# Kernel tuning notes

Measured on AMD Instinct MI355X. Metric: run time of the kernel, lower is better.

The kernel has to match this reference:

```python
import jax, jax.numpy as jnp
import numpy as np

B, L, K, H = 512, 512, 103, 512
I = K + 2  # LSTM input = obs(103) + fed-back pos(2)


def setup_inputs() -> dict:
    key = jax.random.key(0)
    ks = jax.random.split(key, 14)
    s = 0.02
    return {
        "x": jax.random.normal(ks[0], (B, L, K), dtype=jnp.float32),
        "pos": jax.random.normal(ks[1], (B, L, 2), dtype=jnp.float32),
        "hidden_state": jnp.zeros((B, H), dtype=jnp.float32),
        "cell_state": jnp.zeros((B, H), dtype=jnp.float32),
        # LSTM params (PyTorch layout: gates ordered i,f,g,o)
        "W_ih": jax.random.normal(ks[2], (4 * H, I), dtype=jnp.float32) * s,
        "W_hh": jax.random.normal(ks[3], (4 * H, H), dtype=jnp.float32) * s,
        "b_ih": jnp.zeros((4 * H,), dtype=jnp.float32),
        "b_hh": jnp.zeros((4 * H,), dtype=jnp.float32),
        # MLP: H -> 64 -> 16 -> 2, all ReLU
        "W1": jax.random.normal(ks[4], (64, H), dtype=jnp.float32) * s,
        "b1": jnp.zeros((64,), dtype=jnp.float32),
        "W2": jax.random.normal(ks[5], (16, 64), dtype=jnp.float32) * s,
        "b2": jnp.zeros((16,), dtype=jnp.float32),
        "W3": jax.random.normal(ks[6], (2, 16), dtype=jnp.float32) * s,
        "b3": jnp.zeros((2,), dtype=jnp.float32),
    }


def reference(x, pos, hidden_state, cell_state, W_ih, W_hh, b_ih, b_hh,
              W1, b1, W2, b2, W3, b3):
    b = b_ih + b_hh

    def step(carry, x_t):
        h, c, ip = carry  # (B,H),(B,H),(B,2)
        inp = jnp.concatenate([x_t, ip], axis=-1)  # (B, I)
        gates = inp @ W_ih.T + h @ W_hh.T + b      # (B, 4H)
        i, f, g, o = jnp.split(gates, 4, axis=-1)
        c = jax.nn.sigmoid(f) * c + jax.nn.sigmoid(i) * jnp.tanh(g)
        h = jax.nn.sigmoid(o) * jnp.tanh(c)
        y = jax.nn.relu(h @ W1.T + b1)
        y = jax.nn.relu(y @ W2.T + b2)
        y = jax.nn.relu(y @ W3.T + b3)  # (B,2) predicted next pos
        return (h, c, y), y

    xs = jnp.swapaxes(x, 0, 1)  # (L,B,K)
    (h, c, _), ys = jax.lax.scan(step, (hidden_state, cell_state, pos[:, 0, :]), xs)
    predicted_pos = jnp.swapaxes(ys, 0, 1)  # (B,L,2)
    return predicted_pos, h, c
```

## Files before the change

### kernel.cpp

```cpp
#include <hip/hip_runtime.h>

#define NB 512
#define NL 512
#define NK 103
#define NH 512
#define NI 105
#define XROW (NL * NK)

typedef _Float16 half8 __attribute__((ext_vector_type(8)));
typedef _Float16 half4 __attribute__((ext_vector_type(4)));
typedef float floatx4 __attribute__((ext_vector_type(4)));

union U16 { half8 h; unsigned long long u[2]; };

#define XB_STR 136
#define B2_STR 136
#define YST_STR 72
#define Y2_STR 16
#define OFF_XB  0
#define OFF_B2  34816
#define OFF_YST 52224
#define OFF_Y2  61440
#define OFF_FR  63488
#define SMEM_BYTES 65280

#define SPIN_MAX (1 << 20)

#define A_LOAD(p)  __hip_atomic_load((p),  __ATOMIC_RELAXED, __HIP_MEMORY_SCOPE_AGENT)
#define A_STORE(p, v) __hip_atomic_store((p), (v), __ATOMIC_RELAXED, __HIP_MEMORY_SCOPE_AGENT)


__device__ __forceinline__ float fast_sigmoid(float v) {
  v = fminf(fmaxf(v, -30.f), 30.f);
  return __builtin_amdgcn_rcpf(1.f + __expf(-v));
}
__device__ __forceinline__ float fast_tanh(float v) {
  v = fminf(fmaxf(v, -15.f), 15.f);
  float e = __expf(-2.f * v);
  return (1.f - e) * __builtin_amdgcn_rcpf(1.f + e);
}

__global__ void __launch_bounds__(256, 1)
lstm_persist(const float* __restrict__ x, const float* __restrict__ pos,
             const float* __restrict__ h0, const float* __restrict__ c0,
             const float* __restrict__ Wih, const float* __restrict__ Whh,
             const float* __restrict__ bih, const float* __restrict__ bhh,
             const float* __restrict__ W1, const float* __restrict__ b1,
             const float* __restrict__ W2, const float* __restrict__ b2,
             const float* __restrict__ W3, const float* __restrict__ b3,
             float* __restrict__ out, void* __restrict__ ws)
{
  extern __shared__ char smem[];
  _Float16* B2s = (_Float16*)(smem + OFF_B2);
  _Float16* YST = (_Float16*)(smem + OFF_YST);
  _Float16* Y2  = (_Float16*)(smem + OFF_Y2);
  _Float16* HTX = Y2;
  float* FR  = (float*)(smem + OFF_FR);
  float* b1s = FR;
  float* b2s = FR + 64;
  float* w3s = FR + 80;
  float* b3s = FR + 112;
  float* wy0 = FR + 114;
  float* wy1 = FR + 178;
  float* bgs = FR + 242;
  float* ypres = FR + 306;
  volatile int* abflag = (volatile int*)(FR + 440);

  const int tid = threadIdx.x;
  const int g  = blockIdx.x >> 5;
  const int cs = blockIdx.x & 31;
  const int w  = tid >> 6, l = tid & 63;
  const int c16 = l & 15, q = l >> 4;
  const int rh = w >> 1;
  const int ch = w & 1;

  unsigned* flags = (unsigned*)ws;
  char* hbase = (char*)ws + 4096;

  if (tid == 0) *abflag = 0;
  {
    unsigned* xz = (unsigned*)(smem + OFF_XB);
    for (int i = tid; i < 8704; i += 256) xz[i] = 0;
  }
  for (int idx = tid; idx < 64 * 128; idx += 256) {
    int cc = idx >> 7, k = idx & 127;
    int gr = (cc >> 4) * NH + cs * 16 + (cc & 15);
    float v = (k < NK) ? Wih[(size_t)gr * NI + k] : 0.f;
    B2s[cc * B2_STR + k] = (_Float16)v;
  }
  if (tid < 64) {
    int gr = (tid >> 4) * NH + cs * 16 + (tid & 15);
    wy0[tid] = Wih[(size_t)gr * NI + 103];
    wy1[tid] = Wih[(size_t)gr * NI + 104];
    bgs[tid] = bih[gr] + bhh[gr];
    b1s[tid] = b1[tid];
  }
  if (tid < 16) b2s[tid] = b2[tid];
  if (tid < 32) w3s[tid] = W3[tid];
  if (tid < 2)  b3s[tid] = b3[tid];

  {
    const int r = tid >> 2, hb = tid & 3;
    const float* src = h0 + (size_t)(64 * g + r) * NH + cs * 16 + hb * 4;
    union { unsigned long long u; half4 h; } cv;
    cv.h[0] = (_Float16)src[0]; cv.h[1] = (_Float16)src[1];
    cv.h[2] = (_Float16)src[2]; cv.h[3] = (_Float16)src[3];
    A_STORE((unsigned long long*)(hbase + (size_t)cs * 16384
                                  + (size_t)(64 * g + r) * 32 + hb * 8), cv.u);
  }

  half8 bfr[4][16];
  #pragma unroll
  for (int ct = 0; ct < 4; ++ct) {
    const int rown = ch ? (ct * 16 + c16) : (ct * NH + cs * 16 + c16);
    const float* rp = (ch ? W1 : Whh) + (size_t)rown * NH;
    #pragma unroll
    for (int kk = 0; kk < 16; ++kk) {
      const float* p = rp + kk * 32 + q * 8;
      floatx4 f0 = *(const floatx4*)(p);
      floatx4 f1 = *(const floatx4*)(p + 4);
      half8 hv;
      hv[0]=(_Float16)f0[0]; hv[1]=(_Float16)f0[1]; hv[2]=(_Float16)f0[2]; hv[3]=(_Float16)f0[3];
      hv[4]=(_Float16)f1[0]; hv[5]=(_Float16)f1[1]; hv[6]=(_Float16)f1[2]; hv[7]=(_Float16)f1[3];
      bfr[ct][kk] = hv;
    }
  }
  half8 w2f[2];
  if (ch) {
    #pragma unroll
    for (int kk = 0; kk < 2; ++kk) {
      const float* p = W2 + c16 * 64 + kk * 32 + q * 8;
      floatx4 f0 = *(const floatx4*)(p);
      floatx4 f1 = *(const floatx4*)(p + 4);
      half8 hv;
      hv[0]=(_Float16)f0[0]; hv[1]=(_Float16)f0[1]; hv[2]=(_Float16)f0[2]; hv[3]=(_Float16)f0[3];
      hv[4]=(_Float16)f1[0]; hv[5]=(_Float16)f1[1]; hv[6]=(_Float16)f1[2]; hv[7]=(_Float16)f1[3];
      w2f[kk] = hv;
    }
  }
  float cacc[2][4];
  if (!ch) {
    #pragma unroll
    for (int rt = 0; rt < 2; ++rt)
      #pragma unroll
      for (int reg = 0; reg < 4; ++reg)
        cacc[rt][reg] = c0[(size_t)(64 * g + 32 * rh + 16 * rt + q * 4 + reg) * NH + cs * 16 + c16];
  }

  auto xstage = [&](int t1) {
    _Float16* xb = (_Float16*)(smem + OFF_XB) + (size_t)(t1 & 1) * 64 * XB_STR;
    const int row = 32 * rh + (l >> 1);
    const int p = l & 1;
    const float* src = x + (size_t)(64 * g + row) * XROW + (size_t)t1 * NK + p * 52;
    _Float16* dst = xb + row * XB_STR + p * 52;
    const int nfull = p ? 12 : 13;
    for (int cnk = 0; cnk < nfull; ++cnk) {
      float f0 = src[cnk * 4 + 0], f1 = src[cnk * 4 + 1];
      float f2 = src[cnk * 4 + 2], f3 = src[cnk * 4 + 3];
      half4 hv; hv[0]=(_Float16)f0; hv[1]=(_Float16)f1; hv[2]=(_Float16)f2; hv[3]=(_Float16)f3;
      *(half4*)(dst + cnk * 4) = hv;
    }
    if (p) {
      dst[48] = (_Float16)src[48];
      dst[49] = (_Float16)src[49];
      dst[50] = (_Float16)src[50];
    }
  };

  auto fpub = [&](unsigned val) {
    if (tid == 0) A_STORE(flags + ((g << 5) + cs) * 4, val);
  };

  __syncthreads();
  if (!ch) xstage(0);
  __syncthreads();
  fpub(1);

  for (int t = 0; t <= NL; ++t) {
    if (l < 32) {
      unsigned* f = flags + ((g << 5) + l) * 4;
      int spins = 0;
      while (A_LOAD(f) < (unsigned)(t + 1)) {
        if (++spins > SPIN_MAX) { *abflag = 1; break; }
      }
    }

    U16 ar[2][16];
    {
      const char* lb = hbase + (size_t)(t & 1) * 524288
                     + (size_t)(q >> 1) * 16384
                     + (size_t)(64 * g + 32 * rh + c16) * 32 + (q & 1) * 16;
      #pragma unroll
      for (int kk = 0; kk < 16; ++kk) {
        #pragma unroll
        for (int rt = 0; rt < 2; ++rt) {
          const unsigned long long* up =
              (const unsigned long long*)(lb + (size_t)kk * 32768 + rt * 512);
          ar[rt][kk].u[0] = A_LOAD(up);
          ar[rt][kk].u[1] = A_LOAD(up + 1);
        }
      }
    }

    floatx4 acc[4][2] = {};

    if (!ch && t < NL) {
      const _Float16* xb = (const _Float16*)(smem + OFF_XB) + (size_t)(t & 1) * 64 * XB_STR;
      #pragma unroll
      for (int kb = 0; kb < 4; ++kb) {
        half8 ax[2];
        #pragma unroll
        for (int rt = 0; rt < 2; ++rt)
          ax[rt] = *(const half8*)(xb + (32 * rh + 16 * rt + c16) * XB_STR + kb * 32 + q * 8);
        #pragma unroll
        for (int ct = 0; ct < 4; ++ct) {
          half8 bf = *(const half8*)(B2s + (ct * 16 + c16) * B2_STR + kb * 32 + q * 8);
          #pragma unroll
          for (int rt = 0; rt < 2; ++rt)
            acc[ct][rt] = __builtin_amdgcn_mfma_f32_16x16x32_f16(ax[rt], bf, acc[ct][rt], 0, 0, 0);
        }
      }
      if (t + 1 < NL) xstage(t + 1);
    }

    #pragma unroll
    for (int kk = 0; kk < 16; ++kk)
      #pragma unroll
      for (int ct = 0; ct < 4; ++ct) {
        acc[ct][0] = __builtin_amdgcn_mfma_f32_16x16x32_f16(ar[0][kk].h, bfr[ct][kk], acc[ct][0], 0, 0, 0);
        acc[ct][1] = __builtin_amdgcn_mfma_f32_16x16x32_f16(ar[1][kk].h, bfr[ct][kk], acc[ct][1], 0, 0, 0);
      }

    if (ch) {
      if (t == 0) {
        if (l < 32) {
          int row = 32 * rh + l;
          const float* pp = pos + (size_t)(64 * g + row) * (NL * 2);
          ypres[row * 2 + 0] = pp[0];
          ypres[row * 2 + 1] = pp[1];
        }
      } else {
        #pragma unroll
        for (int ct = 0; ct < 4; ++ct)
          #pragma unroll
          for (int rt = 0; rt < 2; ++rt)
            #pragma unroll
            for (int reg = 0; reg < 4; ++reg) {
              int row = 32 * rh + 16 * rt + q * 4 + reg;
              float v = acc[ct][rt][reg] + b1s[ct * 16 + c16];
              YST[row * YST_STR + ct * 16 + c16] = (_Float16)fmaxf(v, 0.f);
            }
        floatx4 a2c[2] = {};
        #pragma unroll
        for (int kk2 = 0; kk2 < 2; ++kk2)
          #pragma unroll
          for (int rt = 0; rt < 2; ++rt) {
            half8 af = *(const half8*)(YST + (32 * rh + 16 * rt + c16) * YST_STR + kk2 * 32 + q * 8);
            a2c[rt] = __builtin_amdgcn_mfma_f32_16x16x32_f16(af, w2f[kk2], a2c[rt], 0, 0, 0);
          }
        #pragma unroll
        for (int rt = 0; rt < 2; ++rt)
          #pragma unroll
          for (int reg = 0; reg < 4; ++reg) {
            int row = 32 * rh + 16 * rt + q * 4 + reg;
            float v = a2c[rt][reg] + b2s[c16];
            Y2[row * Y2_STR + c16] = (_Float16)fmaxf(v, 0.f);
          }
        if (l < 32) {
          int row = 32 * rh + l;
          float y0 = b3s[0], y1 = b3s[1];
          #pragma unroll
          for (int k = 0; k < 16; ++k) {
            float vv = (float)Y2[row * Y2_STR + k];
            y0 += vv * w3s[k];
            y1 += vv * w3s[16 + k];
          }
          y0 = fmaxf(y0, 0.f); y1 = fmaxf(y1, 0.f);
          ypres[row * 2 + 0] = y0;
          ypres[row * 2 + 1] = y1;
          if (cs == 0) {
            float2* op = (float2*)(out + (size_t)(64 * g + row) * (NL * 2) + (size_t)(t - 1) * 2);
            *op = make_float2(y0, y1);
          }
        }
      }
    }
    __syncthreads();
    if (*abflag) return;

    if (!ch && t < NL) {
      #pragma unroll
      for (int rt = 0; rt < 2; ++rt)
        #pragma unroll
        for (int reg = 0; reg < 4; ++reg) {
          int rl = 32 * rh + 16 * rt + q * 4 + reg;
          float yp0 = ypres[rl * 2], yp1 = ypres[rl * 2 + 1];
          float gi = acc[0][rt][reg] + bgs[c16]      + yp0 * wy0[c16]      + yp1 * wy1[c16];
          float gf = acc[1][rt][reg] + bgs[16 + c16] + yp0 * wy0[16 + c16] + yp1 * wy1[16 + c16];
          float gg = acc[2][rt][reg] + bgs[32 + c16] + yp0 * wy0[32 + c16] + yp1 * wy1[32 + c16];
          float go = acc[3][rt][reg] + bgs[48 + c16] + yp0 * wy0[48 + c16] + yp1 * wy1[48 + c16];
          float iv = fast_sigmoid(gi);
          float fv = fast_sigmoid(gf);
          float gv = fast_tanh(gg);
          float ov = fast_sigmoid(go);
          float cn = fv * cacc[rt][reg] + iv * gv;
          cacc[rt][reg] = cn;
          float hn = ov * fast_tanh(cn);
          HTX[rl * 16 + c16] = (_Float16)hn;
          if (t == NL - 1) {
            out[(size_t)(NB * NL * 2) + (size_t)(64 * g + rl) * NH + cs * 16 + c16] = hn;
            out[(size_t)(NB * NL * 2) + (size_t)(NB * NH) + (size_t)(64 * g + rl) * NH + cs * 16 + c16] = cn;
          }
        }
    }

    if (t < NL) {
      __syncthreads();
      {
        const int r = tid >> 2, hb = tid & 3;
        char* dst = hbase + (size_t)((t + 1) & 1) * 524288
                  + (size_t)cs * 16384 + (size_t)(64 * g + r) * 32 + hb * 8;
        unsigned long long v = *(const unsigned long long*)(HTX + r * 16 + hb * 4);
        A_STORE((unsigned long long*)dst, v);
      }
      __syncthreads();
      fpub((unsigned)(t + 2));
    }
  }
}

extern "C" void kernel_launch(void* const* d_in, const int* in_sizes, int n_in,
                              void* d_out, int out_size, void* d_ws, size_t ws_size,
                              hipStream_t stream) {
  (void)in_sizes; (void)n_in; (void)out_size; (void)ws_size;
  const float* x   = (const float*)d_in[0];
  const float* pos = (const float*)d_in[1];
  const float* h0  = (const float*)d_in[2];
  const float* c0  = (const float*)d_in[3];
  const float* Wih = (const float*)d_in[4];
  const float* Whh = (const float*)d_in[5];
  const float* bih = (const float*)d_in[6];
  const float* bhh = (const float*)d_in[7];
  const float* W1  = (const float*)d_in[8];
  const float* b1  = (const float*)d_in[9];
  const float* W2  = (const float*)d_in[10];
  const float* b2  = (const float*)d_in[11];
  const float* W3  = (const float*)d_in[12];
  const float* b3  = (const float*)d_in[13];
  float* out = (float*)d_out;

  hipMemsetAsync(d_ws, 0, 4096, stream);

  void* args[] = { (void*)&x, (void*)&pos, (void*)&h0, (void*)&c0,
                   (void*)&Wih, (void*)&Whh, (void*)&bih, (void*)&bhh,
                   (void*)&W1, (void*)&b1, (void*)&W2, (void*)&b2,
                   (void*)&W3, (void*)&b3, (void*)&out, (void*)&d_ws };

  hipError_t err = hipLaunchCooperativeKernel(
      reinterpret_cast<void*>(lstm_persist),
      dim3(256, 1, 1), dim3(256, 1, 1), args, (unsigned)SMEM_BYTES, stream);
  if (err != hipSuccess) {
    (void)hipGetLastError();
    lstm_persist<<<dim3(256, 1, 1), dim3(256, 1, 1), SMEM_BYTES, stream>>>(
        x, pos, h0, c0, Wih, Whh, bih, bhh, W1, b1, W2, b2, W3, b3, out, d_ws);
  }
}
```

Baseline: 5.453 ms.

## Split LSTM batch into 32-row groups, split-K hidden matmul across wave pairs

Doubles the persistent grid to 512 blocks, each handling 32 batch rows instead of 64, so each block group's per-step work shrinks. Within a block, two waves split the K dimension of the recurrent and W1 matmuls and combine their partial sums through new shared-memory reduction buffers (GG, GM). Publishing h and the step flag now happens from a single wave with an explicit vmcnt wait instead of two extra block barriers. The cost is more blocks spinning on flags, an extra shared-memory reduction per step, and reliance on two blocks fitting per CU for the cooperative launch.

```diff
diff --git a/kernel.cpp b/kernel.cpp
--- a/kernel.cpp
+++ b/kernel.cpp
@@ -16,13 +16,15 @@
 #define XB_STR 136
 #define B2_STR 136
 #define YST_STR 72
-#define Y2_STR 16
 #define OFF_XB  0
-#define OFF_B2  34816
-#define OFF_YST 52224
-#define OFF_Y2  61440
-#define OFF_FR  63488
-#define SMEM_BYTES 65280
+#define OFF_B2  17408
+#define OFF_YST 34816
+#define OFF_Y2  39424
+#define OFF_HTX 40448
+#define OFF_GG  41472
+#define OFF_GM  50176
+#define OFF_FR  58880
+#define SMEM_BYTES 60480
 
 #define SPIN_MAX (1 << 20)
 
@@ -40,7 +42,7 @@
   return (1.f - e) * __builtin_amdgcn_rcpf(1.f + e);
 }
 
-__global__ void __launch_bounds__(256, 1)
+__global__ void __launch_bounds__(256, 2)
 lstm_persist(const float* __restrict__ x, const float* __restrict__ pos,
              const float* __restrict__ h0, const float* __restrict__ c0,
              const float* __restrict__ Wih, const float* __restrict__ Whh,
@@ -54,7 +56,9 @@
   _Float16* B2s = (_Float16*)(smem + OFF_B2);
   _Float16* YST = (_Float16*)(smem + OFF_YST);
   _Float16* Y2  = (_Float16*)(smem + OFF_Y2);
-  _Float16* HTX = Y2;
+  _Float16* HTX = (_Float16*)(smem + OFF_HTX);
+  float* GG = (float*)(smem + OFF_GG);
+  float* GM = (float*)(smem + OFF_GM);
   float* FR  = (float*)(smem + OFF_FR);
   float* b1s = FR;
   float* b2s = FR + 64;
@@ -64,23 +68,23 @@
   float* wy1 = FR + 178;
   float* bgs = FR + 242;
   float* ypres = FR + 306;
-  volatile int* abflag = (volatile int*)(FR + 440);
+  volatile int* abflag = (volatile int*)(FR + 370);
 
   const int tid = threadIdx.x;
   const int g  = blockIdx.x >> 5;
   const int cs = blockIdx.x & 31;
   const int w  = tid >> 6, l = tid & 63;
   const int c16 = l & 15, q = l >> 4;
-  const int rh = w >> 1;
-  const int ch = w & 1;
+  const int pair = w >> 1;
+  const int wv = w & 1;
 
   unsigned* flags = (unsigned*)ws;
-  char* hbase = (char*)ws + 4096;
+  char* hbase = (char*)ws + 8192;
 
   if (tid == 0) *abflag = 0;
   {
     unsigned* xz = (unsigned*)(smem + OFF_XB);
-    for (int i = tid; i < 8704; i += 256) xz[i] = 0;
+    for (int i = tid; i < 4352; i += 256) xz[i] = 0;
   }
   for (int idx = tid; idx < 64 * 128; idx += 256) {
     int cc = idx >> 7, k = idx & 127;
@@ -99,24 +103,24 @@
   if (tid < 32) w3s[tid] = W3[tid];
   if (tid < 2)  b3s[tid] = b3[tid];
 
-  {
+  if (tid < 128) {
     const int r = tid >> 2, hb = tid & 3;
-    const float* src = h0 + (size_t)(64 * g + r) * NH + cs * 16 + hb * 4;
+    const float* src = h0 + (size_t)(32 * g + r) * NH + cs * 16 + hb * 4;
     union { unsigned long long u; half4 h; } cv;
     cv.h[0] = (_Float16)src[0]; cv.h[1] = (_Float16)src[1];
     cv.h[2] = (_Float16)src[2]; cv.h[3] = (_Float16)src[3];
     A_STORE((unsigned long long*)(hbase + (size_t)cs * 16384
-                                  + (size_t)(64 * g + r) * 32 + hb * 8), cv.u);
-  }
-
-  half8 bfr[4][16];
+                                  + (size_t)(32 * g + r) * 32 + hb * 8), cv.u);
+  }
+
+  half8 bfr[4][8];
   #pragma unroll
   for (int ct = 0; ct < 4; ++ct) {
-    const int rown = ch ? (ct * 16 + c16) : (ct * NH + cs * 16 + c16);
-    const float* rp = (ch ? W1 : Whh) + (size_t)rown * NH;
+    const int rown = pair ? (ct * 16 + c16) : (ct * NH + cs * 16 + c16);
+    const float* rp = (pair ? W1 : Whh) + (size_t)rown * NH;
     #pragma unroll
-    for (int kk = 0; kk < 16; ++kk) {
-      const float* p = rp + kk * 32 + q * 8;
+    for (int kk = 0; kk < 8; ++kk) {
+      const float* p = rp + (wv * 8 + kk) * 32 + q * 8;
       floatx4 f0 = *(const floatx4*)(p);
       floatx4 f1 = *(const floatx4*)(p + 4);
       half8 hv;
@@ -126,7 +130,7 @@
     }
   }
   half8 w2f[2];
-  if (ch) {
+  if (w == 2) {
     #pragma unroll
     for (int kk = 0; kk < 2; ++kk) {
       const float* p = W2 + c16 * 64 + kk * 32 + q * 8;
@@ -138,20 +142,18 @@
       w2f[kk] = hv;
     }
   }
-  float cacc[2][4];
-  if (!ch) {
+  float cacc[4];
+  if (pair == 0) {
     #pragma unroll
-    for (int rt = 0; rt < 2; ++rt)
-      #pragma unroll
-      for (int reg = 0; reg < 4; ++reg)
-        cacc[rt][reg] = c0[(size_t)(64 * g + 32 * rh + 16 * rt + q * 4 + reg) * NH + cs * 16 + c16];
+    for (int reg = 0; reg < 4; ++reg)
+      cacc[reg] = c0[(size_t)(32 * g + 16 * wv + q * 4 + reg) * NH + cs * 16 + c16];
   }
 
   auto xstage = [&](int t1) {
-    _Float16* xb = (_Float16*)(smem + OFF_XB) + (size_t)(t1 & 1) * 64 * XB_STR;
-    const int row = 32 * rh + (l >> 1);
+    _Float16* xb = (_Float16*)(smem + OFF_XB) + (size_t)(t1 & 1) * 32 * XB_STR;
+    const int row = l >> 1;
     const int p = l & 1;
-    const float* src = x + (size_t)(64 * g + row) * XROW + (size_t)t1 * NK + p * 52;
+    const float* src = x + (size_t)(32 * g + row) * XROW + (size_t)t1 * NK + p * 52;
     _Float16* dst = xb + row * XB_STR + p * 52;
     const int nfull = p ? 12 : 13;
     for (int cnk = 0; cnk < nfull; ++cnk) {
@@ -167,77 +169,103 @@
     }
   };
 
-  auto fpub = [&](unsigned val) {
-    if (tid == 0) A_STORE(flags + ((g << 5) + cs) * 4, val);
-  };
-
   __syncthreads();
-  if (!ch) xstage(0);
+  if (w == 1) xstage(0);
   __syncthreads();
-  fpub(1);
+  if (tid == 0) A_STORE(flags + ((g << 5) + cs) * 4, 1u);
 
   for (int t = 0; t <= NL; ++t) {
-    if (l < 32) {
-      unsigned* f = flags + ((g << 5) + l) * 4;
-      int spins = 0;
-      while (A_LOAD(f) < (unsigned)(t + 1)) {
-        if (++spins > SPIN_MAX) { *abflag = 1; break; }
-      }
-    }
-
-    U16 ar[2][16];
-    {
-      const char* lb = hbase + (size_t)(t & 1) * 524288
-                     + (size_t)(q >> 1) * 16384
-                     + (size_t)(64 * g + 32 * rh + c16) * 32 + (q & 1) * 16;
+    floatx4 acc[4][2] = {};
+    const bool active = (pair == 1) || (t < NL);
+
+    if (active) {
+      if (l < 16) {
+        unsigned* f = flags + ((g << 5) + wv * 16 + l) * 4;
+        int spins = 0;
+        while (A_LOAD(f) < (unsigned)(t + 1)) {
+          if (++spins > SPIN_MAX) { *abflag = 1; break; }
+        }
+      }
+      U16 ar[2][8];
+      {
+        const char* lb = hbase + (size_t)(t & 1) * 524288
+                       + (size_t)wv * 262144 + (size_t)(q >> 1) * 16384
+                       + (size_t)(32 * g + c16) * 32 + (q & 1) * 16;
+        #pragma unroll
+        for (int kk = 0; kk < 8; ++kk) {
+          #pragma unroll
+          for (int rt = 0; rt < 2; ++rt) {
+            const unsigned long long* up =
+                (const unsigned long long*)(lb + (size_t)kk * 32768 + rt * 512);
+            ar[rt][kk].u[0] = A_LOAD(up);
+            ar[rt][kk].u[1] = A_LOAD(up + 1);
+          }
+        }
+      }
+
+      if (pair == 0 && t < NL) {
+        const _Float16* xb = (const _Float16*)(smem + OFF_XB) + (size_t)(t & 1) * 32 * XB_STR;
+        #pragma unroll
+        for (int kbi = 0; kbi < 2; ++kbi) {
+          const int kb = 2 * wv + kbi;
+          half8 ax[2];
+          #pragma unroll
+          for (int rt = 0; rt < 2; ++rt)
+            ax[rt] = *(const half8*)(xb + (16 * rt + c16) * XB_STR + kb * 32 + q * 8);
+          #pragma unroll
+          for (int ct = 0; ct < 4; ++ct) {
+            half8 bf = *(const half8*)(B2s + (ct * 16 + c16) * B2_STR + kb * 32 + q * 8);
+            #pragma unroll
+            for (int rt = 0; rt < 2; ++rt)
+              acc[ct][rt] = __builtin_amdgcn_mfma_f32_16x16x32_f16(ax[rt], bf, acc[ct][rt], 0, 0, 0);
+          }
+        }
+        if (w == 1 && t + 1 < NL) xstage(t + 1);
+      }
+
       #pragma unroll
-      for (int kk = 0; kk < 16; ++kk) {
-        #pragma unroll
-        for (int rt = 0; rt < 2; ++rt) {
-          const unsigned long long* up =
-              (const unsigned long long*)(lb + (size_t)kk * 32768 + rt * 512);
-          ar[rt][kk].u[0] = A_LOAD(up);
-          ar[rt][kk].u[1] = A_LOAD(up + 1);
-        }
-      }
-    }
-
-    floatx4 acc[4][2] = {};
-
-    if (!ch && t < NL) {
-      const _Float16* xb = (const _Float16*)(smem + OFF_XB) + (size_t)(t & 1) * 64 * XB_STR;
+      for (int kk = 0; kk < 8; ++kk)
+        #pragma unroll
+        for (int ct = 0; ct < 4; ++ct) {
+          acc[ct][0] = __builtin_amdgcn_mfma_f32_16x16x32_f16(ar[0][kk].h, bfr[ct][kk], acc[ct][0], 0, 0, 0);
+          acc[ct][1] = __builtin_amdgcn_mfma_f32_16x16x32_f16(ar[1][kk].h, bfr[ct][kk], acc[ct][1], 0, 0, 0);
+        }
+
+      if (pair == 0) {
+        #pragma unroll
+        for (int ct = 0; ct < 4; ++ct)
+          #pragma unroll
+          for (int reg = 0; reg < 4; ++reg)
+            GG[(1 - wv) * 1088 + ct * 272 + (q * 4 + reg) * 17 + c16] = acc[ct][1 - wv][reg];
+      } else if (wv == 1) {
+        #pragma unroll
+        for (int ct = 0; ct < 4; ++ct)
+          #pragma unroll
+          for (int rt = 0; rt < 2; ++rt)
+            #pragma unroll
+            for (int reg = 0; reg < 4; ++reg)
+              GM[ct * 544 + rt * 272 + (q * 4 + reg) * 17 + c16] = acc[ct][rt][reg];
+      }
+    }
+    __syncthreads();
+    if (*abflag) return;
+
+    float gfull[4][4];
+    if (pair == 0 && t < NL) {
       #pragma unroll
-      for (int kb = 0; kb < 4; ++kb) {
-        half8 ax[2];
-        #pragma unroll
-        for (int rt = 0; rt < 2; ++rt)
-          ax[rt] = *(const half8*)(xb + (32 * rh + 16 * rt + c16) * XB_STR + kb * 32 + q * 8);
-        #pragma unroll
-        for (int ct = 0; ct < 4; ++ct) {
-          half8 bf = *(const half8*)(B2s + (ct * 16 + c16) * B2_STR + kb * 32 + q * 8);
-          #pragma unroll
-          for (int rt = 0; rt < 2; ++rt)
-            acc[ct][rt] = __builtin_amdgcn_mfma_f32_16x16x32_f16(ax[rt], bf, acc[ct][rt], 0, 0, 0);
-        }
-      }
-      if (t + 1 < NL) xstage(t + 1);
-    }
-
-    #pragma unroll
-    for (int kk = 0; kk < 16; ++kk)
-      #pragma unroll
-      for (int ct = 0; ct < 4; ++ct) {
-        acc[ct][0] = __builtin_amdgcn_mfma_f32_16x16x32_f16(ar[0][kk].h, bfr[ct][kk], acc[ct][0], 0, 0, 0);
-        acc[ct][1] = __builtin_amdgcn_mfma_f32_16x16x32_f16(ar[1][kk].h, bfr[ct][kk], acc[ct][1], 0, 0, 0);
-      }
-
-    if (ch) {
+      for (int ct = 0; ct < 4; ++ct)
+        #pragma unroll
+        for (int reg = 0; reg < 4; ++reg)
+          gfull[ct][reg] = acc[ct][wv][reg]
+                         + GG[wv * 1088 + ct * 272 + (q * 4 + reg) * 17 + c16];
+    }
+
+    if (w == 2) {
       if (t == 0) {
         if (l < 32) {
-          int row = 32 * rh + l;
-          const float* pp = pos + (size_t)(64 * g + row) * (NL * 2);
-          ypres[row * 2 + 0] = pp[0];
-          ypres[row * 2 + 1] = pp[1];
+          const float* pp = pos + (size_t)(32 * g + l) * (NL * 2);
+          ypres[l * 2 + 0] = pp[0];
+          ypres[l * 2 + 1] = pp[1];
         }
       } else {
         #pragma unroll
@@ -246,8 +274,10 @@
           for (int rt = 0; rt < 2; ++rt)
             #pragma unroll
             for (int reg = 0; reg < 4; ++reg) {
-              int row = 32 * rh + 16 * rt + q * 4 + reg;
-              float v = acc[ct][rt][reg] + b1s[ct * 16 + c16];
+              int row = 16 * rt + q * 4 + reg;
+              float v = acc[ct][rt][reg]
+                      + GM[ct * 544 + rt * 272 + (q * 4 + reg) * 17 + c16]
+                      + b1s[ct * 16 + c16];
               YST[row * YST_STR + ct * 16 + c16] = (_Float16)fmaxf(v, 0.f);
             }
         floatx4 a2c[2] = {};
@@ -255,76 +285,71 @@
         for (int kk2 = 0; kk2 < 2; ++kk2)
           #pragma unroll
           for (int rt = 0; rt < 2; ++rt) {
-            half8 af = *(const half8*)(YST + (32 * rh + 16 * rt + c16) * YST_STR + kk2 * 32 + q * 8);
+            half8 af = *(const half8*)(YST + (16 * rt + c16) * YST_STR + kk2 * 32 + q * 8);
             a2c[rt] = __builtin_amdgcn_mfma_f32_16x16x32_f16(af, w2f[kk2], a2c[rt], 0, 0, 0);
           }
         #pragma unroll
         for (int rt = 0; rt < 2; ++rt)
           #pragma unroll
           for (int reg = 0; reg < 4; ++reg) {
-            int row = 32 * rh + 16 * rt + q * 4 + reg;
+            int row = 16 * rt + q * 4 + reg;
             float v = a2c[rt][reg] + b2s[c16];
-            Y2[row * Y2_STR + c16] = (_Float16)fmaxf(v, 0.f);
+            Y2[row * 16 + c16] = (_Float16)fmaxf(v, 0.f);
           }
         if (l < 32) {
-          int row = 32 * rh + l;
           float y0 = b3s[0], y1 = b3s[1];
           #pragma unroll
           for (int k = 0; k < 16; ++k) {
-            float vv = (float)Y2[row * Y2_STR + k];
+            float vv = (float)Y2[l * 16 + k];
             y0 += vv * w3s[k];
             y1 += vv * w3s[16 + k];
           }
           y0 = fmaxf(y0, 0.f); y1 = fmaxf(y1, 0.f);
-          ypres[row * 2 + 0] = y0;
-          ypres[row * 2 + 1] = y1;
+          ypres[l * 2 + 0] = y0;
+          ypres[l * 2 + 1] = y1;
           if (cs == 0) {
-            float2* op = (float2*)(out + (size_t)(64 * g + row) * (NL * 2) + (size_t)(t - 1) * 2);
+            float2* op = (float2*)(out + (size_t)(32 * g + l) * (NL * 2) + (size_t)(t - 1) * 2);
             *op = make_float2(y0, y1);
           }
         }
       }
     }
     __syncthreads();
-    if (*abflag) return;
-
-    if (!ch && t < NL) {
+
+    if (pair == 0 && t < NL) {
       #pragma unroll
-      for (int rt = 0; rt < 2; ++rt)
-        #pragma unroll
-        for (int reg = 0; reg < 4; ++reg) {
-          int rl = 32 * rh + 16 * rt + q * 4 + reg;
-          float yp0 = ypres[rl * 2], yp1 = ypres[rl * 2 + 1];
-          float gi = acc[0][rt][reg] + bgs[c16]      + yp0 * wy0[c16]      + yp1 * wy1[c16];
-          float gf = acc[1][rt][reg] + bgs[16 + c16] + yp0 * wy0[16 + c16] + yp1 * wy1[16 + c16];
-          float gg = acc[2][rt][reg] + bgs[32 + c16] + yp0 * wy0[32 + c16] + yp1 * wy1[32 + c16];
-          float go = acc[3][rt][reg] + bgs[48 + c16] + yp0 * wy0[48 + c16] + yp1 * wy1[48 + c16];
-          float iv = fast_sigmoid(gi);
-          float fv = fast_sigmoid(gf);
-          float gv = fast_tanh(gg);
-          float ov = fast_sigmoid(go);
-          float cn = fv * cacc[rt][reg] + iv * gv;
-          cacc[rt][reg] = cn;
-          float hn = ov * fast_tanh(cn);
-          HTX[rl * 16 + c16] = (_Float16)hn;
-          if (t == NL - 1) {
-            out[(size_t)(NB * NL * 2) + (size_t)(64 * g + rl) * NH + cs * 16 + c16] = hn;
-            out[(size_t)(NB * NL * 2) + (size_t)(NB * NH) + (size_t)(64 * g + rl) * NH + cs * 16 + c16] = cn;
-          }
-        }
-    }
-
-    if (t < NL) {
-      __syncthreads();
-      {
-        const int r = tid >> 2, hb = tid & 3;
-        char* dst = hbase + (size_t)((t + 1) & 1) * 524288
-                  + (size_t)cs * 16384 + (size_t)(64 * g + r) * 32 + hb * 8;
-        unsigned long long v = *(const unsigned long long*)(HTX + r * 16 + hb * 4);
-        A_STORE((unsigned long long*)dst, v);
-      }
-      __syncthreads();
-      fpub((unsigned)(t + 2));
+      for (int reg = 0; reg < 4; ++reg) {
+        const int rl = 16 * wv + q * 4 + reg;
+        float yp0 = ypres[rl * 2], yp1 = ypres[rl * 2 + 1];
+        float gi = gfull[0][reg] + bgs[c16]      + yp0 * wy0[c16]      + yp1 * wy1[c16];
+        float gf = gfull[1][reg] + bgs[16 + c16] + yp0 * wy0[16 + c16] + yp1 * wy1[16 + c16];
+        float gg = gfull[2][reg] + bgs[32 + c16] + yp0 * wy0[32 + c16] + yp1 * wy1[32 + c16];
+        float go = gfull[3][reg] + bgs[48 + c16] + yp0 * wy0[48 + c16] + yp1 * wy1[48 + c16];
+        float iv = fast_sigmoid(gi);
+        float fv = fast_sigmoid(gf);
+        float gv = fast_tanh(gg);
+        float ov = fast_sigmoid(go);
+        float cn = fv * cacc[reg] + iv * gv;
+        cacc[reg] = cn;
+        float hn = ov * fast_tanh(cn);
+        HTX[rl * 16 + c16] = (_Float16)hn;
+        if (t == NL - 1) {
+          out[(size_t)(NB * NL * 2) + (size_t)(32 * g + rl) * NH + cs * 16 + c16] = hn;
+          out[(size_t)(NB * NL * 2) + (size_t)(NB * NH) + (size_t)(32 * g + rl) * NH + cs * 16 + c16] = cn;
+        }
+      }
+    }
+    __syncthreads();
+
+    if (t < NL && w == 0) {
+      const int row = l >> 1, part = l & 1;
+      const unsigned long long* src = (const unsigned long long*)(HTX + row * 16 + part * 8);
+      char* dst = hbase + (size_t)((t + 1) & 1) * 524288
+                + (size_t)cs * 16384 + (size_t)(32 * g + row) * 32 + part * 16;
+      A_STORE((unsigned long long*)dst, src[0]);
+      A_STORE((unsigned long long*)dst + 1, src[1]);
+      asm volatile("s_waitcnt vmcnt(0)" ::: "memory");
+      if (l == 0) A_STORE(flags + ((g << 5) + cs) * 4, (unsigned)(t + 2));
     }
   }
 }
@@ -349,7 +374,7 @@
   const float* b3  = (const float*)d_in[13];
   float* out = (float*)d_out;
 
-  hipMemsetAsync(d_ws, 0, 4096, stream);
+  hipMemsetAsync(d_ws, 0, 8192, stream);
 
   void* args[] = { (void*)&x, (void*)&pos, (void*)&h0, (void*)&c0,
                    (void*)&Wih, (void*)&Whh, (void*)&bih, (void*)&bhh,
@@ -358,10 +383,10 @@
 
   hipError_t err = hipLaunchCooperativeKernel(
       reinterpret_cast<void*>(lstm_persist),
-      dim3(256, 1, 1), dim3(256, 1, 1), args, (unsigned)SMEM_BYTES, stream);
+      dim3(512, 1, 1), dim3(256, 1, 1), args, (unsigned)SMEM_BYTES, stream);
   if (err != hipSuccess) {
     (void)hipGetLastError();
-    lstm_persist<<<dim3(256, 1, 1), dim3(256, 1, 1), SMEM_BYTES, stream>>>(
+    lstm_persist<<<dim3(512, 1, 1), dim3(256, 1, 1), SMEM_BYTES, stream>>>(
         x, pos, h0, c0, Wih, Whh, bih, bhh, W1, b1, W2, b2, W3, b3, out, d_ws);
   }
 }
```

After: 12.51 ms. 129% more time.

## Streamline cross-block h publication and flag polling in persistent LSTM

Applied to the files above, without the earlier changes.

Moves HTX into its own shared-memory region so it no longer aliases Y2. The second block-wide barrier after the h store is removed: wave 0 alone writes each row's 32 bytes, waits on vmcnt, then sets the step flag. Flags are padded to 64-byte spacing, each wave staggers which flags it polls first, and spinning threads back off with s_sleep. The goal is to cut cross-workgroup synchronisation latency per timestep. The risks are that one wave now does all the global stores, that dynamic shared memory grows past 64 KB, and that store visibility ordering relies only on a relaxed store after vmcnt(0).

```diff
diff --git a/kernel.cpp b/kernel.cpp
--- a/kernel.cpp
+++ b/kernel.cpp
@@ -21,8 +21,9 @@
 #define OFF_B2  34816
 #define OFF_YST 52224
 #define OFF_Y2  61440
-#define OFF_FR  63488
-#define SMEM_BYTES 65280
+#define OFF_HTX 63488
+#define OFF_FR  65536
+#define SMEM_BYTES 67328
 
 #define SPIN_MAX (1 << 20)
 
@@ -54,7 +55,7 @@
   _Float16* B2s = (_Float16*)(smem + OFF_B2);
   _Float16* YST = (_Float16*)(smem + OFF_YST);
   _Float16* Y2  = (_Float16*)(smem + OFF_Y2);
-  _Float16* HTX = Y2;
+  _Float16* HTX = (_Float16*)(smem + OFF_HTX);
   float* FR  = (float*)(smem + OFF_FR);
   float* b1s = FR;
   float* b2s = FR + 64;
@@ -75,7 +76,7 @@
   const int ch = w & 1;
 
   unsigned* flags = (unsigned*)ws;
-  char* hbase = (char*)ws + 4096;
+  char* hbase = (char*)ws + 16384;
 
   if (tid == 0) *abflag = 0;
   {
@@ -167,21 +168,19 @@
     }
   };
 
-  auto fpub = [&](unsigned val) {
-    if (tid == 0) A_STORE(flags + ((g << 5) + cs) * 4, val);
-  };
-
   __syncthreads();
   if (!ch) xstage(0);
   __syncthreads();
-  fpub(1);
+  if (tid == 0) A_STORE(flags + ((g << 5) + cs) * 16, 1u);
 
   for (int t = 0; t <= NL; ++t) {
     if (l < 32) {
-      unsigned* f = flags + ((g << 5) + l) * 4;
+      const int fi = (l + 8 * w) & 31;
+      unsigned* f = flags + ((g << 5) + fi) * 16;
       int spins = 0;
       while (A_LOAD(f) < (unsigned)(t + 1)) {
         if (++spins > SPIN_MAX) { *abflag = 1; break; }
+        if ((spins & 63) == 0) __builtin_amdgcn_s_sleep(1);
       }
     }
 
@@ -316,15 +315,17 @@
 
     if (t < NL) {
       __syncthreads();
-      {
-        const int r = tid >> 2, hb = tid & 3;
+      if (w == 0) {
+        const unsigned long long* src = (const unsigned long long*)(HTX + l * 16);
         char* dst = hbase + (size_t)((t + 1) & 1) * 524288
-                  + (size_t)cs * 16384 + (size_t)(64 * g + r) * 32 + hb * 8;
-        unsigned long long v = *(const unsigned long long*)(HTX + r * 16 + hb * 4);
-        A_STORE((unsigned long long*)dst, v);
-      }
-      __syncthreads();
-      fpub((unsigned)(t + 2));
+                  + (size_t)cs * 16384 + (size_t)(64 * g + l) * 32;
+        A_STORE((unsigned long long*)dst + 0, src[0]);
+        A_STORE((unsigned long long*)dst + 1, src[1]);
+        A_STORE((unsigned long long*)dst + 2, src[2]);
+        A_STORE((unsigned long long*)dst + 3, src[3]);
+        asm volatile("s_waitcnt vmcnt(0)" ::: "memory");
+        if (l == 0) A_STORE(flags + ((g << 5) + cs) * 16, (unsigned)(t + 2));
+      }
     }
   }
 }
@@ -349,7 +350,10 @@
   const float* b3  = (const float*)d_in[13];
   float* out = (float*)d_out;
 
-  hipMemsetAsync(d_ws, 0, 4096, stream);
+  hipMemsetAsync(d_ws, 0, 16384, stream);
+
+  hipFuncSetAttribute(reinterpret_cast<const void*>(lstm_persist),
+                      hipFuncAttributeMaxDynamicSharedMemorySize, SMEM_BYTES);
 
   void* args[] = { (void*)&x, (void*)&pos, (void*)&h0, (void*)&c0,
                    (void*)&Wih, (void*)&Whh, (void*)&bih, (void*)&bhh,
```

New measurement: 5.484 ms. Within noise of the previous version (+0.6%).
